# Kernel tuning notes

Measured on AMD Instinct MI355X. Metric: run time of the kernel, lower is better.

## Reference

```python
import jax, jax.numpy as jnp
import numpy as np

D_MODEL = 1024
GEOM_DIM = 32
CLAMP_VALUE = 10.0


def setup_inputs() -> dict:
    key = jax.random.key(0)
    k1, k2, k3 = jax.random.split(key, 3)
    B, N = 4, 2048
    H = jax.random.normal(k1, (B, N, D_MODEL), dtype=jnp.float32)
    B_prev = jax.random.normal(k2, (B, N, N), dtype=jnp.float32)
    # geom_proj weight, init std=0.001 as in the torch module
    W = jax.random.normal(k3, (GEOM_DIM, D_MODEL), dtype=jnp.float32) * 0.001
    alpha = jnp.asarray(1.0, dtype=jnp.float32)
    beta = jnp.asarray(0.05, dtype=jnp.float32)
    return {"H": H, "B_prev": B_prev, "W": W, "alpha": alpha, "beta": beta}


def reference(H, B_prev, W, alpha, beta):
    # Low-rank projection: G [B, N, geom_dim]
    G = jnp.einsum("bnd,kd->bnk", H, W)
    G_sq = jnp.sum(G * G, axis=-1)  # [B, N]
    # Pairwise squared distance: [B, N, N]
    gram = jnp.einsum("bik,bjk->bij", G, G)
    dist = G_sq[:, :, None] + G_sq[:, None, :] - 2.0 * gram
    dist = jnp.maximum(dist, 0.0)
    # EMA bias update with clamp
    B_next = alpha * B_prev - beta * dist
    B_next = jnp.clip(B_next, -CLAMP_VALUE, CLAMP_VALUE)
    return B_next
```

## Files before the change

### kernel.cpp

```cpp
#include <hip/hip_runtime.h>


typedef __attribute__((ext_vector_type(8))) short short8;
typedef __attribute__((ext_vector_type(4))) float floatx4;

static __device__ __forceinline__ short bf16_bits(float f) {
    union { float f; unsigned int u; } v; v.f = f;
    unsigned int u = v.u;
    u += 0x7FFFu + ((u >> 16) & 1u);
    return (short)(u >> 16);
}

static __device__ __forceinline__ float bf16_to_f32(unsigned short h) {
    union { unsigned int u; float f; } v; v.u = ((unsigned int)h) << 16;
    return v.f;
}

__global__ __launch_bounds__(256) void k1_proj(const float* __restrict__ H,
                                               const float* __restrict__ W,
                                               unsigned short* __restrict__ G,
                                               float* __restrict__ Q) {
    const int blk  = blockIdx.x;
    const int t    = threadIdx.x;
    const int w    = t >> 6;
    const int lane = t & 63;
    const int m    = lane & 15;
    const int quad = lane >> 4;

    const float* hrow  = H + ((long)blk * 16 + m) * 1024;
    const float* wrow0 = W + (long)m * 1024;
    const float* wrow1 = W + (long)(m + 16) * 1024;

    const int kq = w * 256 + quad * 8;

    floatx4 acc0 = {0.f, 0.f, 0.f, 0.f};
    floatx4 acc1 = {0.f, 0.f, 0.f, 0.f};

    float4 a0  = *(const float4*)(hrow  + kq);
    float4 a1  = *(const float4*)(hrow  + kq + 4);
    float4 b00 = *(const float4*)(wrow0 + kq);
    float4 b01 = *(const float4*)(wrow0 + kq + 4);
    float4 b10 = *(const float4*)(wrow1 + kq);
    float4 b11 = *(const float4*)(wrow1 + kq + 4);

    #pragma unroll
    for (int step = 0; step < 8; ++step) {
        float4 na0, na1, nb00, nb01, nb10, nb11;
        if (step < 7) {
            const int nk = kq + (step + 1) * 32;
            na0  = *(const float4*)(hrow  + nk);
            na1  = *(const float4*)(hrow  + nk + 4);
            nb00 = *(const float4*)(wrow0 + nk);
            nb01 = *(const float4*)(wrow0 + nk + 4);
            nb10 = *(const float4*)(wrow1 + nk);
            nb11 = *(const float4*)(wrow1 + nk + 4);
        }
        short8 af, bf0, bf1;
        af[0] = bf16_bits(a0.x);  af[1] = bf16_bits(a0.y);
        af[2] = bf16_bits(a0.z);  af[3] = bf16_bits(a0.w);
        af[4] = bf16_bits(a1.x);  af[5] = bf16_bits(a1.y);
        af[6] = bf16_bits(a1.z);  af[7] = bf16_bits(a1.w);
        bf0[0] = bf16_bits(b00.x); bf0[1] = bf16_bits(b00.y);
        bf0[2] = bf16_bits(b00.z); bf0[3] = bf16_bits(b00.w);
        bf0[4] = bf16_bits(b01.x); bf0[5] = bf16_bits(b01.y);
        bf0[6] = bf16_bits(b01.z); bf0[7] = bf16_bits(b01.w);
        bf1[0] = bf16_bits(b10.x); bf1[1] = bf16_bits(b10.y);
        bf1[2] = bf16_bits(b10.z); bf1[3] = bf16_bits(b10.w);
        bf1[4] = bf16_bits(b11.x); bf1[5] = bf16_bits(b11.y);
        bf1[6] = bf16_bits(b11.z); bf1[7] = bf16_bits(b11.w);

        acc0 = __builtin_amdgcn_mfma_f32_16x16x32_bf16(af, bf0, acc0, 0, 0, 0);
        acc1 = __builtin_amdgcn_mfma_f32_16x16x32_bf16(af, bf1, acc1, 0, 0, 0);

        if (step < 7) { a0 = na0; a1 = na1; b00 = nb00; b01 = nb01; b10 = nb10; b11 = nb11; }
    }

    __shared__ float red[4][16][32];
    #pragma unroll
    for (int r = 0; r < 4; ++r) {
        red[w][quad * 4 + r][m]      = acc0[r];
        red[w][quad * 4 + r][m + 16] = acc1[r];
    }
    __syncthreads();
    for (int e = t; e < 512; e += 256) {
        const int mm = e >> 5, nn = e & 31;
        float v = red[0][mm][nn] + red[1][mm][nn] + red[2][mm][nn] + red[3][mm][nn];
        const unsigned short hb = (unsigned short)bf16_bits(v);
        G[(long)(blk * 16 + mm) * 32 + nn] = hb;
        red[0][mm][nn] = bf16_to_f32(hb);
    }
    __syncthreads();
    if (t < 16) {
        float s = 0.f;
        #pragma unroll
        for (int nn = 0; nn < 32; ++nn) { const float v = red[0][t][nn]; s += v * v; }
        Q[blk * 16 + t] = s;
    }
}

__global__ __launch_bounds__(256) void k2_update(const float* __restrict__ Bp,
                                                 const unsigned short* __restrict__ G,
                                                 const float* __restrict__ Q,
                                                 const float* __restrict__ alphap,
                                                 const float* __restrict__ betap,
                                                 float* __restrict__ out) {
    __shared__ short sGi[64 * 40];
    __shared__ short sGj[128 * 40];
    __shared__ float sQi[64];
    __shared__ float sQj[128];

    const int b  = blockIdx.z;
    const int i0 = blockIdx.y * 64;
    const int j0 = blockIdx.x * 128;
    const int t  = threadIdx.x;

    const short* Gg = (const short*)G;
    {
        const int r = t >> 2, c = t & 3;
        *(short8*)&sGi[r * 40 + c * 8] =
            *(const short8*)&Gg[(long)(b * 2048 + i0 + r) * 32 + c * 8];
    }
    #pragma unroll
    for (int l = 0; l < 2; ++l) {
        const int f = t + l * 256;
        const int r = f >> 2, c = f & 3;
        *(short8*)&sGj[r * 40 + c * 8] =
            *(const short8*)&Gg[(long)(b * 2048 + j0 + r) * 32 + c * 8];
    }
    if (t < 64)       sQi[t]      = Q[b * 2048 + i0 + t];
    else if (t < 192) sQj[t - 64] = Q[b * 2048 + j0 + (t - 64)];
    __syncthreads();

    const int w    = t >> 6;
    const int lane = t & 63;
    const int m    = lane & 15;
    const int quad = lane >> 4;

    const short8 af = *(const short8*)&sGi[(w * 16 + m) * 40 + quad * 8];
    floatx4 acc[8];
    #pragma unroll
    for (int jt = 0; jt < 8; ++jt) {
        const short8 bf = *(const short8*)&sGj[(jt * 16 + m) * 40 + quad * 8];
        floatx4 z = {0.f, 0.f, 0.f, 0.f};
        acc[jt] = __builtin_amdgcn_mfma_f32_16x16x32_bf16(af, bf, z, 0, 0, 0);
    }

    const float alpha = alphap[0];
    const float beta  = betap[0];

    float qj[8];
    #pragma unroll
    for (int jt = 0; jt < 8; ++jt) qj[jt] = sQj[jt * 16 + m];

    const long base = (long)b * 2048 * 2048;
    #pragma unroll
    for (int r = 0; r < 4; ++r) {
        const int i = i0 + w * 16 + quad * 4 + r;
        const float qi = sQi[w * 16 + quad * 4 + r];
        const float* bprow = Bp  + base + (long)i * 2048 + j0 + m;
        float*       orow  = out + base + (long)i * 2048 + j0 + m;
        float bv[8];
        #pragma unroll
        for (int jt = 0; jt < 8; ++jt) bv[jt] = bprow[jt * 16];
        #pragma unroll
        for (int jt = 0; jt < 8; ++jt) {
            float d = qi + qj[jt] - 2.f * acc[jt][r];
            d = fmaxf(d, 0.f);
            orow[jt * 16] = fminf(fmaxf(alpha * bv[jt] - beta * d, -10.f), 10.f);
        }
    }
}

extern "C" void kernel_launch(void* const* d_in, const int* in_sizes, int n_in,
                              void* d_out, int out_size, void* d_ws, size_t ws_size,
                              hipStream_t stream) {
    const float* H     = (const float*)d_in[0];
    const float* Bp    = (const float*)d_in[1];
    const float* W     = (const float*)d_in[2];
    const float* alpha = (const float*)d_in[3];
    const float* beta  = (const float*)d_in[4];
    float* out = (float*)d_out;

    unsigned short* G = (unsigned short*)d_ws;
    float* Q = (float*)((char*)d_ws + 8192 * 32 * 2);

    k1_proj<<<512, 256, 0, stream>>>(H, W, G, Q);

    dim3 g2(16, 32, 4);
    k2_update<<<g2, 256, 0, stream>>>(Bp, G, Q, alpha, beta, out);
}
```

Before: 158.2 us.

## Vectorize B_prev/output access via transposed MFMA and pre-cast W to bf16

The update kernel swaps the MFMA operands so each lane holds four consecutive j values of one row. B_prev loads and output stores become float4 accesses, and the B_prev loads are issued before the G staging to overlap latency. The projection kernel now stages a bf16-converted H tile in shared memory. W is cast to bf16 once by a new small kernel, which removes repeated per-block conversion work at the cost of an extra launch and more shared memory.

Measured after the change: 158.6 us. Within noise of the previous version (+0.2%).

```diff
diff --git a/kernel.cpp b/kernel.cpp
--- a/kernel.cpp
+++ b/kernel.cpp
@@ -2,6 +2,7 @@
 
 
 typedef __attribute__((ext_vector_type(8))) short short8;
+typedef __attribute__((ext_vector_type(4))) short short4v;
 typedef __attribute__((ext_vector_type(4))) float floatx4;
 
 static __device__ __forceinline__ short bf16_bits(float f) {
@@ -16,8 +17,18 @@
     return v.f;
 }
 
+__global__ __launch_bounds__(256) void k0_wcast(const float* __restrict__ W,
+                                                short* __restrict__ Wb) {
+    const int f = blockIdx.x * 256 + threadIdx.x;
+    const float4 v = *(const float4*)(W + (long)f * 4);
+    short4v s;
+    s[0] = bf16_bits(v.x); s[1] = bf16_bits(v.y);
+    s[2] = bf16_bits(v.z); s[3] = bf16_bits(v.w);
+    *(short4v*)(Wb + (long)f * 4) = s;
+}
+
 __global__ __launch_bounds__(256) void k1_proj(const float* __restrict__ H,
-                                               const float* __restrict__ W,
+                                               const short* __restrict__ Wb,
                                                unsigned short* __restrict__ G,
                                                float* __restrict__ Q) {
     const int blk  = blockIdx.x;
@@ -27,52 +38,46 @@
     const int m    = lane & 15;
     const int quad = lane >> 4;
 
-    const float* hrow  = H + ((long)blk * 16 + m) * 1024;
-    const float* wrow0 = W + (long)m * 1024;
-    const float* wrow1 = W + (long)(m + 16) * 1024;
+    __shared__ short sH[16 * 1032];
+
+    const float* Hb = H + (long)blk * 16384;
+    #pragma unroll
+    for (int it = 0; it < 8; ++it) {
+        const int f  = t + it * 256;
+        const int r  = f >> 7;
+        const int c8 = f & 127;
+        const float4 v0 = *(const float4*)(Hb + r * 1024 + c8 * 8);
+        const float4 v1 = *(const float4*)(Hb + r * 1024 + c8 * 8 + 4);
+        short8 sv;
+        sv[0] = bf16_bits(v0.x); sv[1] = bf16_bits(v0.y);
+        sv[2] = bf16_bits(v0.z); sv[3] = bf16_bits(v0.w);
+        sv[4] = bf16_bits(v1.x); sv[5] = bf16_bits(v1.y);
+        sv[6] = bf16_bits(v1.z); sv[7] = bf16_bits(v1.w);
+        *(short8*)&sH[r * 1032 + c8 * 8] = sv;
+    }
+    __syncthreads();
 
     const int kq = w * 256 + quad * 8;
+    const short* wb0 = Wb + (long)m * 1024 + kq;
+    const short* wb1 = Wb + (long)(m + 16) * 1024 + kq;
 
     floatx4 acc0 = {0.f, 0.f, 0.f, 0.f};
     floatx4 acc1 = {0.f, 0.f, 0.f, 0.f};
 
-    float4 a0  = *(const float4*)(hrow  + kq);
-    float4 a1  = *(const float4*)(hrow  + kq + 4);
-    float4 b00 = *(const float4*)(wrow0 + kq);
-    float4 b01 = *(const float4*)(wrow0 + kq + 4);
-    float4 b10 = *(const float4*)(wrow1 + kq);
-    float4 b11 = *(const float4*)(wrow1 + kq + 4);
-
-    #pragma unroll
-    for (int step = 0; step < 8; ++step) {
-        float4 na0, na1, nb00, nb01, nb10, nb11;
-        if (step < 7) {
-            const int nk = kq + (step + 1) * 32;
-            na0  = *(const float4*)(hrow  + nk);
-            na1  = *(const float4*)(hrow  + nk + 4);
-            nb00 = *(const float4*)(wrow0 + nk);
-            nb01 = *(const float4*)(wrow0 + nk + 4);
-            nb10 = *(const float4*)(wrow1 + nk);
-            nb11 = *(const float4*)(wrow1 + nk + 4);
-        }
-        short8 af, bf0, bf1;
-        af[0] = bf16_bits(a0.x);  af[1] = bf16_bits(a0.y);
-        af[2] = bf16_bits(a0.z);  af[3] = bf16_bits(a0.w);
-        af[4] = bf16_bits(a1.x);  af[5] = bf16_bits(a1.y);
-        af[6] = bf16_bits(a1.z);  af[7] = bf16_bits(a1.w);
-        bf0[0] = bf16_bits(b00.x); bf0[1] = bf16_bits(b00.y);
-        bf0[2] = bf16_bits(b00.z); bf0[3] = bf16_bits(b00.w);
-        bf0[4] = bf16_bits(b01.x); bf0[5] = bf16_bits(b01.y);
-        bf0[6] = bf16_bits(b01.z); bf0[7] = bf16_bits(b01.w);
-        bf1[0] = bf16_bits(b10.x); bf1[1] = bf16_bits(b10.y);
-        bf1[2] = bf16_bits(b10.z); bf1[3] = bf16_bits(b10.w);
-        bf1[4] = bf16_bits(b11.x); bf1[5] = bf16_bits(b11.y);
-        bf1[6] = bf16_bits(b11.z); bf1[7] = bf16_bits(b11.w);
-
-        acc0 = __builtin_amdgcn_mfma_f32_16x16x32_bf16(af, bf0, acc0, 0, 0, 0);
-        acc1 = __builtin_amdgcn_mfma_f32_16x16x32_bf16(af, bf1, acc1, 0, 0, 0);
-
-        if (step < 7) { a0 = na0; a1 = na1; b00 = nb00; b01 = nb01; b10 = nb10; b11 = nb11; }
+    short8 b0 = *(const short8*)wb0;
+    short8 b1 = *(const short8*)wb1;
+
+    #pragma unroll
+    for (int s = 0; s < 8; ++s) {
+        short8 nb0, nb1;
+        if (s < 7) {
+            nb0 = *(const short8*)(wb0 + (s + 1) * 32);
+            nb1 = *(const short8*)(wb1 + (s + 1) * 32);
+        }
+        const short8 af = *(const short8*)&sH[m * 1032 + kq + s * 32];
+        acc0 = __builtin_amdgcn_mfma_f32_16x16x32_bf16(af, b0, acc0, 0, 0, 0);
+        acc1 = __builtin_amdgcn_mfma_f32_16x16x32_bf16(af, b1, acc1, 0, 0, 0);
+        if (s < 7) { b0 = nb0; b1 = nb1; }
     }
 
     __shared__ float red[4][16][32];
@@ -113,6 +118,17 @@
     const int i0 = blockIdx.y * 64;
     const int j0 = blockIdx.x * 128;
     const int t  = threadIdx.x;
+    const int w    = t >> 6;
+    const int lane = t & 63;
+    const int m    = lane & 15;
+    const int quad = lane >> 4;
+
+    const int i = i0 + w * 16 + m;
+    const long rowoff = ((long)b * 2048 + i) * 2048 + j0;
+    const float4* bp4 = (const float4*)(Bp + rowoff);
+    float4 bv[8];
+    #pragma unroll
+    for (int jt = 0; jt < 8; ++jt) bv[jt] = bp4[jt * 4 + quad];
 
     const short* Gg = (const short*)G;
     {
@@ -131,43 +147,46 @@
     else if (t < 192) sQj[t - 64] = Q[b * 2048 + j0 + (t - 64)];
     __syncthreads();
 
-    const int w    = t >> 6;
-    const int lane = t & 63;
-    const int m    = lane & 15;
-    const int quad = lane >> 4;
-
-    const short8 af = *(const short8*)&sGi[(w * 16 + m) * 40 + quad * 8];
+    const short8 bfi = *(const short8*)&sGi[(w * 16 + m) * 40 + quad * 8];
     floatx4 acc[8];
     #pragma unroll
     for (int jt = 0; jt < 8; ++jt) {
-        const short8 bf = *(const short8*)&sGj[(jt * 16 + m) * 40 + quad * 8];
+        const short8 afj = *(const short8*)&sGj[(jt * 16 + m) * 40 + quad * 8];
         floatx4 z = {0.f, 0.f, 0.f, 0.f};
-        acc[jt] = __builtin_amdgcn_mfma_f32_16x16x32_bf16(af, bf, z, 0, 0, 0);
+        acc[jt] = __builtin_amdgcn_mfma_f32_16x16x32_bf16(afj, bfi, z, 0, 0, 0);
     }
 
     const float alpha = alphap[0];
     const float beta  = betap[0];
-
-    float qj[8];
-    #pragma unroll
-    for (int jt = 0; jt < 8; ++jt) qj[jt] = sQj[jt * 16 + m];
-
-    const long base = (long)b * 2048 * 2048;
-    #pragma unroll
-    for (int r = 0; r < 4; ++r) {
-        const int i = i0 + w * 16 + quad * 4 + r;
-        const float qi = sQi[w * 16 + quad * 4 + r];
-        const float* bprow = Bp  + base + (long)i * 2048 + j0 + m;
-        float*       orow  = out + base + (long)i * 2048 + j0 + m;
-        float bv[8];
-        #pragma unroll
-        for (int jt = 0; jt < 8; ++jt) bv[jt] = bprow[jt * 16];
-        #pragma unroll
-        for (int jt = 0; jt < 8; ++jt) {
-            float d = qi + qj[jt] - 2.f * acc[jt][r];
-            d = fmaxf(d, 0.f);
-            orow[jt * 16] = fminf(fmaxf(alpha * bv[jt] - beta * d, -10.f), 10.f);
-        }
+    const float qi = sQi[w * 16 + m];
+    float4* o4 = (float4*)(out + rowoff);
+
+    #pragma unroll
+    for (int jt = 0; jt < 8; ++jt) {
+        const float4 qjv = *(const float4*)&sQj[jt * 16 + quad * 4];
+        const float4 bvv = bv[jt];
+        float4 ov;
+        {
+            float d = qi + qjv.x - 2.f * acc[jt][0];
+            d = fmaxf(d, 0.f);
+            ov.x = fminf(fmaxf(alpha * bvv.x - beta * d, -10.f), 10.f);
+        }
+        {
+            float d = qi + qjv.y - 2.f * acc[jt][1];
+            d = fmaxf(d, 0.f);
+            ov.y = fminf(fmaxf(alpha * bvv.y - beta * d, -10.f), 10.f);
+        }
+        {
+            float d = qi + qjv.z - 2.f * acc[jt][2];
+            d = fmaxf(d, 0.f);
+            ov.z = fminf(fmaxf(alpha * bvv.z - beta * d, -10.f), 10.f);
+        }
+        {
+            float d = qi + qjv.w - 2.f * acc[jt][3];
+            d = fmaxf(d, 0.f);
+            ov.w = fminf(fmaxf(alpha * bvv.w - beta * d, -10.f), 10.f);
+        }
+        o4[jt * 4 + quad] = ov;
     }
 }
 
@@ -182,9 +201,11 @@
     float* out = (float*)d_out;
 
     unsigned short* G = (unsigned short*)d_ws;
-    float* Q = (float*)((char*)d_ws + 8192 * 32 * 2);
-
-    k1_proj<<<512, 256, 0, stream>>>(H, W, G, Q);
+    float* Q  = (float*)((char*)d_ws + 8192 * 32 * 2);
+    short* Wb = (short*)((char*)d_ws + 8192 * 32 * 2 + 8192 * 4);
+
+    k0_wcast<<<32, 256, 0, stream>>>(W, Wb);
+    k1_proj<<<512, 256, 0, stream>>>(H, Wb, G, Q);
 
     dim3 g2(16, 32, 4);
     k2_update<<<g2, 256, 0, stream>>>(Bp, G, Q, alpha, beta, out);
```
